# Optimization experiments

Measured on AMD Instinct MI355X. Metric: run time of the kernel, lower is better.

## Reference

```python
import jax, jax.numpy as jnp
import numpy as np

N = 8192          # num nodes
F = 256           # feature_size
D = 128           # graph_embedding_size
E = 262144        # num edges (avg degree 32)
SLOPE = 0.2       # cfg.negativeslope
NEG_INF = -9e15   # matches torch's -9000000000000000.0 mask value


def setup_inputs() -> dict:
    key = jax.random.key(0)
    k1, k2, k3, k4 = jax.random.split(key, 4)
    X = jax.random.normal(k1, (N, F), dtype=jnp.float32)
    edge_index = jax.random.randint(k2, (2, E), 0, N, dtype=jnp.int64)
    # glorot init for Ws, xavier_uniform(gain=1.414) for a
    lim_ws = np.sqrt(6.0 / (F + D)).astype(np.float32)
    Ws = jax.random.uniform(k3, (F, D), jnp.float32, -lim_ws, lim_ws)
    lim_a = (1.414 * np.sqrt(6.0 / (2 * D + 1))).astype(np.float32)
    a = jax.random.uniform(k4, (2 * D, 1), jnp.float32, -lim_a, lim_a)
    return {"edge_index": edge_index, "X": X, "Ws": Ws, "a": a}


def reference(edge_index, X, Ws, a):
    # dense adjacency mask from edge list (sparse_coo_tensor(...).to_dense())
    adj = jnp.zeros((N, N), jnp.float32).at[edge_index[0], edge_index[1]].set(1.0)
    Wh = X @ Ws                                   # [N, D]
    # GAT-style score: Wh1_i + Wh2_j, then leaky relu
    e = jax.nn.leaky_relu(Wh @ a[:D] + (Wh @ a[D:]).T, SLOPE)  # [N, N]
    scores = jnp.where(adj > 0, e, NEG_INF)
    att = jax.nn.softmax(scores, axis=1)          # masked row softmax
    return jax.nn.elu(att @ Wh)                   # [N, D]
```

## Files before the change

kernel.cpp:

```cpp
#include <hip/hip_runtime.h>
#include <math.h>

#define N_NODES 8192
#define FDIM 256
#define DDIM 128
#define SLOPE 0.2f
#define ELLW 128

__device__ __forceinline__ unsigned short f2bf(float f) {
    unsigned u = __float_as_uint(f);
    u += 0x7fffu + ((u >> 16) & 1u);
    return (unsigned short)(u >> 16);
}
__device__ __forceinline__ float bf2f(unsigned short h) {
    return __uint_as_float(((unsigned)h) << 16);
}

__global__ __launch_bounds__(256) void build_ell(const int* __restrict__ edge, int E,
                                                 unsigned* __restrict__ cnt,
                                                 unsigned* __restrict__ ell) {
    int e = blockIdx.x * blockDim.x + threadIdx.x;
    if (e >= E) return;
    int r = edge[e];
    int c = edge[E + e];
    unsigned slot = atomicAdd(&cnt[r], 1u);
    if (slot < ELLW) ell[(size_t)r * ELLW + slot] = (unsigned)c;
}

__global__ __launch_bounds__(256) void gemm_wh_fused(const float* __restrict__ X,
                                                     const float* __restrict__ Ws,
                                                     const float* __restrict__ a,
                                                     unsigned short* __restrict__ WhB,
                                                     float* __restrict__ s1,
                                                     float* __restrict__ s2,
                                                     unsigned* __restrict__ cnt) {
    __shared__ float4 xs4[32 * 64];
    __shared__ float4 ws4[64 * 32];
    int t = threadIdx.x;
    int row0 = blockIdx.x * 32;

    if (blockIdx.x < 32) cnt[blockIdx.x * 256 + t] = 0u;

    const float4* Xg = (const float4*)(X + (size_t)row0 * FDIM);
    for (int i = t; i < 2048; i += 256) xs4[i] = Xg[i];

    int rg = t >> 5, cg = t & 31;
    float4 acc[4];
#pragma unroll
    for (int rr = 0; rr < 4; rr++) acc[rr] = make_float4(0.f, 0.f, 0.f, 0.f);

    for (int c = 0; c < 4; c++) {
        __syncthreads();
        const float4* Wg = (const float4*)(Ws + (size_t)c * 64 * DDIM);
        for (int i = t; i < 2048; i += 256) ws4[i] = Wg[i];
        __syncthreads();
#pragma unroll 2
        for (int kk = 0; kk < 64; kk += 4) {
            float4 xv[4], wv[4];
#pragma unroll
            for (int rr = 0; rr < 4; rr++)
                xv[rr] = xs4[(rg * 4 + rr) * 64 + c * 16 + (kk >> 2)];
#pragma unroll
            for (int q = 0; q < 4; q++)
                wv[q] = ws4[(kk + q) * 32 + cg];
#pragma unroll
            for (int rr = 0; rr < 4; rr++) {
                const float* xf = (const float*)&xv[rr];
#pragma unroll
                for (int q = 0; q < 4; q++) {
                    float x = xf[q];
                    acc[rr].x = fmaf(x, wv[q].x, acc[rr].x);
                    acc[rr].y = fmaf(x, wv[q].y, acc[rr].y);
                    acc[rr].z = fmaf(x, wv[q].z, acc[rr].z);
                    acc[rr].w = fmaf(x, wv[q].w, acc[rr].w);
                }
            }
        }
    }

#pragma unroll
    for (int rr = 0; rr < 4; rr++) {
        ushort4 h;
        h.x = f2bf(acc[rr].x); h.y = f2bf(acc[rr].y);
        h.z = f2bf(acc[rr].z); h.w = f2bf(acc[rr].w);
        *(ushort4*)(WhB + (size_t)(row0 + rg * 4 + rr) * DDIM + cg * 4) = h;
    }

    float4 a1 = ((const float4*)a)[cg];
    float4 a2 = ((const float4*)a)[32 + cg];
#pragma unroll
    for (int rr = 0; rr < 4; rr++) {
        float p1 = acc[rr].x * a1.x + acc[rr].y * a1.y + acc[rr].z * a1.z + acc[rr].w * a1.w;
        float p2 = acc[rr].x * a2.x + acc[rr].y * a2.y + acc[rr].z * a2.z + acc[rr].w * a2.w;
        for (int o = 16; o; o >>= 1) {
            p1 += __shfl_xor(p1, o, 32);
            p2 += __shfl_xor(p2, o, 32);
        }
        if (cg == 0) {
            s1[row0 + rg * 4 + rr] = p1;
            s2[row0 + rg * 4 + rr] = p2;
        }
    }
}

__global__ __launch_bounds__(256) void row_wave_k(const unsigned* __restrict__ cnt,
                                                  const unsigned* __restrict__ ell,
                                                  const float* __restrict__ s1v,
                                                  const float* __restrict__ s2v,
                                                  const unsigned short* __restrict__ WhB,
                                                  float* __restrict__ out) {
    __shared__ unsigned bmw[4][256];
    __shared__ float    pl[4][ELLW];
    __shared__ unsigned jl[4][ELLW];

    int w = threadIdx.x >> 6, lane = threadIdx.x & 63;
    int i = blockIdx.x * 4 + w;
    const ushort2* WhB2 = (const ushort2*)WhB;

    ((uint4*)bmw[w])[lane] = make_uint4(0u, 0u, 0u, 0u);
    unsigned deg = cnt[i];
    if (deg > ELLW) deg = ELLW;
    __syncthreads();

    if (deg == 0u) {
        float sx = 0.f, sy = 0.f;
        for (int rr = 0; rr < N_NODES; rr++) {
            ushort2 u = WhB2[(size_t)rr * 64 + lane];
            sx += bf2f(u.x); sy += bf2f(u.y);
        }
        sx *= (1.0f / N_NODES); sy *= (1.0f / N_NODES);
        sx = sx > 0.f ? sx : __expf(sx) - 1.f;
        sy = sy > 0.f ? sy : __expf(sy) - 1.f;
        ((float2*)out)[(size_t)i * 64 + lane] = make_float2(sx, sy);
        return;
    }

    const unsigned* erow = ell + (size_t)i * ELLW;
    unsigned j0 = 0u, j1 = 0u;
    bool v0 = false, v1 = false;
    if (lane < (int)deg) j0 = erow[lane];
    if (lane + 64 < (int)deg) j1 = erow[lane + 64];
    if (lane < (int)deg) {
        unsigned m = 1u << (j0 & 31);
        v0 = !(atomicOr(&bmw[w][j0 >> 5], m) & m);
    }
    if (lane + 64 < (int)deg) {
        unsigned m = 1u << (j1 & 31);
        v1 = !(atomicOr(&bmw[w][j1 >> 5], m) & m);
    }

    float s1 = s1v[i];
    float e0 = -3e38f, e1 = -3e38f;
    if (v0) { float e = s1 + s2v[j0]; e0 = e > 0.f ? e : SLOPE * e; }
    if (v1) { float e = s1 + s2v[j1]; e1 = e > 0.f ? e : SLOPE * e; }

    float mx = fmaxf(e0, e1);
    for (int o = 32; o; o >>= 1) mx = fmaxf(mx, __shfl_xor(mx, o, 64));

    float p0 = v0 ? __expf(e0 - mx) : 0.f;
    float p1 = v1 ? __expf(e1 - mx) : 0.f;
    float s = p0 + p1;
    for (int o = 32; o; o >>= 1) s += __shfl_xor(s, o, 64);
    float inv = 1.0f / s;

    pl[w][lane] = p0;      jl[w][lane] = j0;
    pl[w][lane + 64] = p1; jl[w][lane + 64] = j1;

    float ax = 0.f, ay = 0.f;
#pragma unroll 8
    for (unsigned n = 0; n < deg; ++n) {
        float p = pl[w][n];
        unsigned j = jl[w][n];
        ushort2 u = WhB2[(size_t)j * 64 + lane];
        ax = fmaf(p, bf2f(u.x), ax);
        ay = fmaf(p, bf2f(u.y), ay);
    }
    ax *= inv; ay *= inv;
    ax = ax > 0.f ? ax : __expf(ax) - 1.f;
    ay = ay > 0.f ? ay : __expf(ay) - 1.f;
    ((float2*)out)[(size_t)i * 64 + lane] = make_float2(ax, ay);
}

extern "C" void kernel_launch(void* const* d_in, const int* in_sizes, int n_in,
                              void* d_out, int out_size, void* d_ws, size_t ws_size,
                              hipStream_t stream) {
    const int*   edge = (const int*)d_in[0];
    const float* X    = (const float*)d_in[1];
    const float* Ws   = (const float*)d_in[2];
    const float* a    = (const float*)d_in[3];
    float*       out  = (float*)d_out;
    int E = in_sizes[0] / 2;

    char* ws = (char*)d_ws;
    size_t off = 0;
    unsigned*       cnt = (unsigned*)(ws + off); off += 32 * 1024;
    unsigned*       ell = (unsigned*)(ws + off); off += (size_t)N_NODES * ELLW * 4;
    float*          s1  = (float*)(ws + off);    off += N_NODES * 4;
    float*          s2  = (float*)(ws + off);    off += N_NODES * 4;
    unsigned short* WhB = (unsigned short*)(ws + off); off += (size_t)N_NODES * DDIM * 2;

    gemm_wh_fused<<<N_NODES / 32, 256, 0, stream>>>(X, Ws, a, WhB, s1, s2, cnt);
    build_ell<<<(E + 255) / 256, 256, 0, stream>>>(edge, E, cnt, ell);
    row_wave_k<<<N_NODES / 4, 256, 0, stream>>>(cnt, ell, s1, s2, WhB, out);
}
```

Before: 43.36 us.

## Replace FP32 SIMT GEMM with split-bf16 MFMA GEMM and weight prep kernel

Result: faster. 40.73 us (-6.1%).

```diff
diff --git a/kernel.cpp b/kernel.cpp
--- a/kernel.cpp
+++ b/kernel.cpp
@@ -7,6 +7,9 @@
 #define SLOPE 0.2f
 #define ELLW 128
 
+typedef __attribute__((ext_vector_type(8))) short bf16x8;
+typedef __attribute__((ext_vector_type(4))) float f32x4;
+
 __device__ __forceinline__ unsigned short f2bf(float f) {
     unsigned u = __float_as_uint(f);
     u += 0x7fffu + ((u >> 16) & 1u);
@@ -14,6 +17,40 @@
 }
 __device__ __forceinline__ float bf2f(unsigned short h) {
     return __uint_as_float(((unsigned)h) << 16);
+}
+
+__global__ __launch_bounds__(256) void prep_k(const float* __restrict__ Ws,
+                                              unsigned short* __restrict__ Wthi,
+                                              unsigned short* __restrict__ Wtlo,
+                                              unsigned* __restrict__ cnt) {
+    int b = blockIdx.x, t = threadIdx.x;
+    cnt[b * 256 + t] = 0u;
+    if (b >= 8) return;
+    __shared__ float ls[32][129];
+    int k0 = b * 32;
+#pragma unroll
+    for (int i = 0; i < 16; i++) {
+        int lin = t + 256 * i;
+        int kk = lin >> 7, col = lin & 127;
+        ls[kk][col] = Ws[(size_t)(k0 + kk) * DDIM + col];
+    }
+    __syncthreads();
+    int col = t >> 1, part = t & 1;
+#pragma unroll
+    for (int g = 0; g < 4; g++) {
+        ushort4 h, l;
+        float v0 = ls[part * 16 + g * 4 + 0][col];
+        float v1 = ls[part * 16 + g * 4 + 1][col];
+        float v2 = ls[part * 16 + g * 4 + 2][col];
+        float v3 = ls[part * 16 + g * 4 + 3][col];
+        h.x = f2bf(v0); l.x = f2bf(v0 - bf2f(h.x));
+        h.y = f2bf(v1); l.y = f2bf(v1 - bf2f(h.y));
+        h.z = f2bf(v2); l.z = f2bf(v2 - bf2f(h.z));
+        h.w = f2bf(v3); l.w = f2bf(v3 - bf2f(h.w));
+        size_t o = (size_t)col * FDIM + k0 + part * 16 + g * 4;
+        *(ushort4*)(Wthi + o) = h;
+        *(ushort4*)(Wtlo + o) = l;
+    }
 }
 
 __global__ __launch_bounds__(256) void build_ell(const int* __restrict__ edge, int E,
@@ -27,79 +64,88 @@
     if (slot < ELLW) ell[(size_t)r * ELLW + slot] = (unsigned)c;
 }
 
-__global__ __launch_bounds__(256) void gemm_wh_fused(const float* __restrict__ X,
-                                                     const float* __restrict__ Ws,
-                                                     const float* __restrict__ a,
-                                                     unsigned short* __restrict__ WhB,
-                                                     float* __restrict__ s1,
-                                                     float* __restrict__ s2,
-                                                     unsigned* __restrict__ cnt) {
-    __shared__ float4 xs4[32 * 64];
-    __shared__ float4 ws4[64 * 32];
+__global__ __launch_bounds__(256) void gemm_mfma2(const float* __restrict__ X,
+                                                  const unsigned short* __restrict__ Wthi,
+                                                  const unsigned short* __restrict__ Wtlo,
+                                                  const float* __restrict__ a,
+                                                  unsigned short* __restrict__ WhB,
+                                                  float* __restrict__ s1,
+                                                  float* __restrict__ s2) {
+    __shared__ unsigned short Ah[16 * 264], Al[16 * 264];
+    __shared__ unsigned short Bh[128 * 72], Bl[128 * 72];
+    __shared__ float ps1[64], ps2[64];
     int t = threadIdx.x;
-    int row0 = blockIdx.x * 32;
-
-    if (blockIdx.x < 32) cnt[blockIdx.x * 256 + t] = 0u;
+    int w = t >> 6, lane = t & 63, lr = lane & 15, kg = lane >> 4;
+    int row0 = blockIdx.x * 16;
+    int colbase = w * 32;
 
     const float4* Xg = (const float4*)(X + (size_t)row0 * FDIM);
-    for (int i = t; i < 2048; i += 256) xs4[i] = Xg[i];
-
-    int rg = t >> 5, cg = t & 31;
-    float4 acc[4];
-#pragma unroll
-    for (int rr = 0; rr < 4; rr++) acc[rr] = make_float4(0.f, 0.f, 0.f, 0.f);
+#pragma unroll
+    for (int i = 0; i < 4; i++) {
+        int lin = t + 256 * i;
+        int r = lin >> 6, q = lin & 63;
+        float4 v = Xg[r * 64 + q];
+        ushort4 h, l;
+        h.x = f2bf(v.x); l.x = f2bf(v.x - bf2f(h.x));
+        h.y = f2bf(v.y); l.y = f2bf(v.y - bf2f(h.y));
+        h.z = f2bf(v.z); l.z = f2bf(v.z - bf2f(h.z));
+        h.w = f2bf(v.w); l.w = f2bf(v.w - bf2f(h.w));
+        *(ushort4*)(Ah + r * 264 + q * 4) = h;
+        *(ushort4*)(Al + r * 264 + q * 4) = l;
+    }
+
+    f32x4 acc0 = (f32x4){0.f, 0.f, 0.f, 0.f};
+    f32x4 acc1 = (f32x4){0.f, 0.f, 0.f, 0.f};
 
     for (int c = 0; c < 4; c++) {
+        if (c) __syncthreads();
+#pragma unroll
+        for (int i = 0; i < 4; i++) {
+            int lin = t + 256 * i;
+            int col = lin >> 3, q = lin & 7;
+            size_t src = (size_t)col * FDIM + c * 64 + q * 8;
+            *(uint4*)(Bh + col * 72 + q * 8) = *(const uint4*)(Wthi + src);
+            *(uint4*)(Bl + col * 72 + q * 8) = *(const uint4*)(Wtlo + src);
+        }
         __syncthreads();
-        const float4* Wg = (const float4*)(Ws + (size_t)c * 64 * DDIM);
-        for (int i = t; i < 2048; i += 256) ws4[i] = Wg[i];
-        __syncthreads();
-#pragma unroll 2
-        for (int kk = 0; kk < 64; kk += 4) {
-            float4 xv[4], wv[4];
-#pragma unroll
-            for (int rr = 0; rr < 4; rr++)
-                xv[rr] = xs4[(rg * 4 + rr) * 64 + c * 16 + (kk >> 2)];
-#pragma unroll
-            for (int q = 0; q < 4; q++)
-                wv[q] = ws4[(kk + q) * 32 + cg];
-#pragma unroll
-            for (int rr = 0; rr < 4; rr++) {
-                const float* xf = (const float*)&xv[rr];
-#pragma unroll
-                for (int q = 0; q < 4; q++) {
-                    float x = xf[q];
-                    acc[rr].x = fmaf(x, wv[q].x, acc[rr].x);
-                    acc[rr].y = fmaf(x, wv[q].y, acc[rr].y);
-                    acc[rr].z = fmaf(x, wv[q].z, acc[rr].z);
-                    acc[rr].w = fmaf(x, wv[q].w, acc[rr].w);
-                }
-            }
-        }
-    }
-
-#pragma unroll
-    for (int rr = 0; rr < 4; rr++) {
-        ushort4 h;
-        h.x = f2bf(acc[rr].x); h.y = f2bf(acc[rr].y);
-        h.z = f2bf(acc[rr].z); h.w = f2bf(acc[rr].w);
-        *(ushort4*)(WhB + (size_t)(row0 + rg * 4 + rr) * DDIM + cg * 4) = h;
-    }
-
-    float4 a1 = ((const float4*)a)[cg];
-    float4 a2 = ((const float4*)a)[32 + cg];
-#pragma unroll
-    for (int rr = 0; rr < 4; rr++) {
-        float p1 = acc[rr].x * a1.x + acc[rr].y * a1.y + acc[rr].z * a1.z + acc[rr].w * a1.w;
-        float p2 = acc[rr].x * a2.x + acc[rr].y * a2.y + acc[rr].z * a2.z + acc[rr].w * a2.w;
-        for (int o = 16; o; o >>= 1) {
-            p1 += __shfl_xor(p1, o, 32);
-            p2 += __shfl_xor(p2, o, 32);
-        }
-        if (cg == 0) {
-            s1[row0 + rg * 4 + rr] = p1;
-            s2[row0 + rg * 4 + rr] = p2;
-        }
+#pragma unroll
+        for (int ks = 0; ks < 2; ks++) {
+            int ko = c * 64 + ks * 32;
+            bf16x8 ahi = *(bf16x8*)(Ah + lr * 264 + ko + kg * 8);
+            bf16x8 alo = *(bf16x8*)(Al + lr * 264 + ko + kg * 8);
+            int c0 = colbase + lr, c1 = colbase + 16 + lr;
+            bf16x8 bh0 = *(bf16x8*)(Bh + c0 * 72 + ks * 32 + kg * 8);
+            bf16x8 bl0 = *(bf16x8*)(Bl + c0 * 72 + ks * 32 + kg * 8);
+            bf16x8 bh1 = *(bf16x8*)(Bh + c1 * 72 + ks * 32 + kg * 8);
+            bf16x8 bl1 = *(bf16x8*)(Bl + c1 * 72 + ks * 32 + kg * 8);
+            acc0 = __builtin_amdgcn_mfma_f32_16x16x32_bf16(ahi, bh0, acc0, 0, 0, 0);
+            acc0 = __builtin_amdgcn_mfma_f32_16x16x32_bf16(ahi, bl0, acc0, 0, 0, 0);
+            acc0 = __builtin_amdgcn_mfma_f32_16x16x32_bf16(alo, bh0, acc0, 0, 0, 0);
+            acc1 = __builtin_amdgcn_mfma_f32_16x16x32_bf16(ahi, bh1, acc1, 0, 0, 0);
+            acc1 = __builtin_amdgcn_mfma_f32_16x16x32_bf16(ahi, bl1, acc1, 0, 0, 0);
+            acc1 = __builtin_amdgcn_mfma_f32_16x16x32_bf16(alo, bh1, acc1, 0, 0, 0);
+        }
+    }
+
+#pragma unroll
+    for (int r = 0; r < 4; r++) {
+        int row = row0 + kg * 4 + r;
+        int c0 = colbase + lr, c1 = colbase + 16 + lr;
+        float v0 = acc0[r], v1 = acc1[r];
+        WhB[(size_t)row * DDIM + c0] = f2bf(v0);
+        WhB[(size_t)row * DDIM + c1] = f2bf(v1);
+        float q1 = v0 * a[c0] + v1 * a[c1];
+        float q2 = v0 * a[DDIM + c0] + v1 * a[DDIM + c1];
+        for (int o = 1; o < 16; o <<= 1) {
+            q1 += __shfl_xor(q1, o, 16);
+            q2 += __shfl_xor(q2, o, 16);
+        }
+        if (lr == 0) { ps1[w * 16 + kg * 4 + r] = q1; ps2[w * 16 + kg * 4 + r] = q2; }
+    }
+    __syncthreads();
+    if (t < 16) {
+        s1[row0 + t] = (ps1[t] + ps1[16 + t]) + (ps1[32 + t] + ps1[48 + t]);
+        s2[row0 + t] = (ps2[t] + ps2[16 + t]) + (ps2[32 + t] + ps2[48 + t]);
     }
 }
 
@@ -193,13 +239,16 @@
 
     char* ws = (char*)d_ws;
     size_t off = 0;
-    unsigned*       cnt = (unsigned*)(ws + off); off += 32 * 1024;
-    unsigned*       ell = (unsigned*)(ws + off); off += (size_t)N_NODES * ELLW * 4;
-    float*          s1  = (float*)(ws + off);    off += N_NODES * 4;
-    float*          s2  = (float*)(ws + off);    off += N_NODES * 4;
-    unsigned short* WhB = (unsigned short*)(ws + off); off += (size_t)N_NODES * DDIM * 2;
-
-    gemm_wh_fused<<<N_NODES / 32, 256, 0, stream>>>(X, Ws, a, WhB, s1, s2, cnt);
+    unsigned*       cnt  = (unsigned*)(ws + off); off += 32 * 1024;
+    unsigned*       ell  = (unsigned*)(ws + off); off += (size_t)N_NODES * ELLW * 4;
+    float*          s1   = (float*)(ws + off);    off += N_NODES * 4;
+    float*          s2   = (float*)(ws + off);    off += N_NODES * 4;
+    unsigned short* WhB  = (unsigned short*)(ws + off); off += (size_t)N_NODES * DDIM * 2;
+    unsigned short* Wthi = (unsigned short*)(ws + off); off += (size_t)FDIM * DDIM * 2;
+    unsigned short* Wtlo = (unsigned short*)(ws + off); off += (size_t)FDIM * DDIM * 2;
+
+    prep_k<<<32, 256, 0, stream>>>(Ws, Wthi, Wtlo, cnt);
     build_ell<<<(E + 255) / 256, 256, 0, stream>>>(edge, E, cnt, ell);
+    gemm_mfma2<<<N_NODES / 16, 256, 0, stream>>>(X, Wthi, Wtlo, a, WhB, s1, s2);
     row_wave_k<<<N_NODES / 4, 256, 0, stream>>>(cnt, ell, s1, s2, WhB, out);
 }
```
